# Kernel optimization log

Measured on AMD Instinct MI355X. Metric: run time of the kernel, lower is better.

## Reference

```python
import jax, jax.numpy as jnp
import numpy as np

RF = 8.0            # reduction_factor
NITER = 3           # k_means_iterations
FWHM = 128.0
TEMP_S = 0.066
TEMP_T = 0.033
MAX_DIST = 4.0
SIGMA2 = (FWHM / 2.355) ** 2


def _norm(x):
    # F.normalize(p=2, dim=-1) with eps=1e-12
    n = jnp.linalg.norm(x, axis=-1, keepdims=True)
    return x / jnp.maximum(n, 1e-12)


def _resize_axis(x, axis, out_size):
    # Linear resample along one axis with align_corners=False half-pixel
    # convention; equivalent to identity-affine grid_sample (coords stay
    # in-bounds for downsampling, so reflection padding never triggers).
    S = x.shape[axis]
    src = (jnp.arange(out_size, dtype=jnp.float32) + 0.5) * (S / out_size) - 0.5
    i0 = jnp.floor(src)
    w = src - i0
    i0c = jnp.clip(i0.astype(jnp.int32), 0, S - 1)
    i1c = jnp.clip(i0c + 1, 0, S - 1)
    x0 = jnp.take(x, i0c, axis=axis)
    x1 = jnp.take(x, i1c, axis=axis)
    shp = [1] * x.ndim
    shp[axis] = out_size
    w = w.reshape(shp)
    return x0 * (1.0 - w) + x1 * w


def _sample(emb, coord, reduction, jitter=None):
    # reduced size computed from ORIGINAL shape (before jitter crop)
    reduced = [max(int(s // reduction), 1) for s in emb.shape[2:]]
    if jitter is not None:
        j = jitter
        emb = emb[:, :, j[0]:emb.shape[2] - j[1], j[2]:emb.shape[3] - j[3], j[4]:emb.shape[4] - j[5]]
        coord = coord[:, :, j[0]:coord.shape[2] - j[1], j[2]:coord.shape[3] - j[3], j[4]:coord.shape[4] - j[5]]
    for ax, r in zip((2, 3, 4), reduced):
        emb = _resize_axis(emb, ax, r)
        coord = _resize_axis(coord, ax, r)
    b, c = emb.shape[:2]
    emb_flat = emb.reshape(b, c, -1).transpose(0, 2, 1)  # b n c
    return emb_flat, coord  # coord kept 5D: b 3 h w d


def _sqdist(cx, cy):
    # squared pairwise distance between flattened coord volumes: (b, Nx, Ny)
    b = cx.shape[0]
    x = cx.reshape(b, 3, -1)
    y = cy.reshape(b, 3, -1)
    d = x[:, :, :, None] - y[:, :, None, :]
    return jnp.sum(d * d, axis=1)


def _cluster(emb_p, coord_p, emb_t, coord_t):
    emb_t_n = _norm(emb_t)
    emb_p_n = _norm(emb_p)
    b = emb_t.shape[0]
    hp, wp, dp = coord_p.shape[2:]
    coord_t_flat = coord_t.reshape(b, 3, -1).transpose(0, 2, 1)  # b n 3
    for _ in range(NITER):
        sim = jax.nn.softmax(jnp.einsum('bnc,bpc->bnp', emb_t_n, emb_p_n) / TEMP_T, axis=-1)
        w = sim * jnp.exp(-_sqdist(coord_t, coord_p) / (2.0 * SIGMA2))
        denom = jnp.sum(w, axis=1)[:, :, None]  # b p 1
        emb_p = jnp.einsum('bnp,bnc->bpc', w, emb_t) / denom
        emb_p_n = _norm(emb_p)
        cp = jnp.einsum('bnp,bnc->bpc', w, coord_t_flat) / denom  # b p 3
        coord_p = cp.transpose(0, 2, 1).reshape(b, 3, hp, wp, dp)
    sim = jax.nn.softmax(jnp.einsum('bnc,bpc->bnp', emb_t_n, emb_p_n) / TEMP_T, axis=-1)
    w = sim * jnp.exp(-_sqdist(coord_t, coord_p) / (2.0 * SIGMA2))
    return emb_p, coord_p, w


def _assign(emb_z, coord_z, coord_t, emb_p, sim_t_p):
    emb_z_n = _norm(emb_z)
    emb_p_n = _norm(emb_p)
    # nearest-teacher assignment (non-differentiable in torch too)
    d = jnp.sqrt(_sqdist(jax.lax.stop_gradient(coord_z), jax.lax.stop_gradient(coord_t)))  # b Nz Nt
    pos_min = jnp.min(d, axis=-1)
    idx = jnp.argmin(d, axis=-1)                       # b Nz
    mask = (pos_min <= MAX_DIST).astype(emb_z.dtype)    # b Nz
    sim_soft = jax.nn.softmax(jnp.einsum('bnc,bpc->bnp', emb_z_n, emb_p_n) / TEMP_S, axis=-1)
    assignment = jnp.take_along_axis(sim_t_p, idx[:, :, None], axis=1)  # b Nz P
    logterm = jnp.clip(jnp.log(sim_soft + 1e-16), -1000.0, 0.0)
    rows = -jnp.sum(assignment * logterm, axis=-1)      # b Nz
    return jnp.sum(rows * mask, axis=1) / jnp.sum(mask, axis=1)  # (b,)


def setup_inputs() -> dict:
    key = jax.random.key(0)
    k1, k2 = jax.random.split(key)
    B, C, H, W, D = 2, 64, 80, 80, 80
    emb_s = jax.random.normal(k1, (B, C, H, W, D), dtype=jnp.float32)
    emb_t = jax.random.normal(k2, (B, C, H, W, D), dtype=jnp.float32)
    ax = jnp.arange(H, dtype=jnp.float32)
    mesh = jnp.stack(jnp.meshgrid(ax, ax, ax, indexing='ij'), axis=0)  # 3 h w d
    coord = jnp.broadcast_to(mesh[None], (B, 3, H, W, D)).astype(jnp.float32)
    return {"emb_s": emb_s, "emb_t": emb_t, "coord_s": coord, "coord_t": coord}


def reference(emb_s, emb_t, coord_s, coord_t):
    # jitter (torch: randint(0, ceil(rf), 6) under no_grad) -> static ints
    jit = np.random.default_rng(0).integers(0, int(np.ceil(RF)), 6)
    emb_p0, coord_p0 = _sample(emb_t, coord_t, RF * 2)
    emb_ts, coord_ts = _sample(emb_t, coord_t, RF)
    emb_ss, coord_ss = _sample(emb_s, coord_s, RF, jitter=jit)
    emb_p, coord_p, sim_t_p = _cluster(emb_p0, coord_p0, emb_ts, coord_ts)
    per_b = _assign(emb_ss, coord_ss, coord_ts, emb_p, sim_t_p)
    return jnp.mean(per_b)
```

## Files before the change

kernel.cpp:

```cpp
#include <hip/hip_runtime.h>
#include <stdint.h>
#include <stddef.h>


namespace {

constexpr int kB = 2;
constexpr int kNT = 1000, kNP = 125, kNZ = 1000;
constexpr float kTempT = 0.033f, kTempS = 0.066f;
constexpr double kSig2 = (128.0 / 2.355) * (128.0 / 2.355);
constexpr float kTwoSig2 = (float)(2.0 * kSig2);

struct Pcg64 {
  __uint128_t state, inc;
  static __uint128_t mult() {
    return (((__uint128_t)2549297995355413924ULL) << 64) | 4865540595714422341ULL;
  }
  void step() { state = state * mult() + inc; }
  void seed(__uint128_t initstate, __uint128_t initseq) {
    state = 0; inc = (initseq << 1) | 1; step(); state += initstate; step();
  }
  uint64_t next64() {
    step();
    uint64_t xo = (uint64_t)(state >> 64) ^ (uint64_t)state;
    unsigned rot = (unsigned)((uint64_t)(state >> 122) & 63u);
    return (xo >> rot) | (xo << ((64u - rot) & 63u));
  }
};

static inline uint32_t ss_hashmix(uint32_t v, uint32_t& hc) {
  v ^= hc; hc *= 0x931e8875u; v *= hc; v ^= v >> 16; return v;
}
static inline uint32_t ss_mix(uint32_t x, uint32_t y) {
  uint32_t r = (0xca01f9ddu * x) ^ (0x4973f715u * y);
  r ^= r >> 16; return r;
}

static void numpy_jitter_seed0(int jit[6]) {
  uint32_t pool[4];
  uint32_t hc = 0x43b0d7e5u;
  for (int i = 0; i < 4; ++i) pool[i] = ss_hashmix(0u, hc);
  for (int s = 0; s < 4; ++s)
    for (int d = 0; d < 4; ++d)
      if (s != d) pool[d] = ss_mix(pool[d], ss_hashmix(pool[s], hc));
  uint32_t w32[8];
  uint32_t hb = 0x8b51f9ddu;
  for (int i = 0; i < 8; ++i) {
    uint32_t dv = pool[i & 3];
    dv ^= hb; hb *= 0x58f38dedu; dv *= hb; dv ^= dv >> 16;
    w32[i] = dv;
  }
  uint64_t w64[4];
  for (int i = 0; i < 4; ++i)
    w64[i] = (uint64_t)w32[2 * i] | ((uint64_t)w32[2 * i + 1] << 32);
  Pcg64 rng;
  rng.seed((((__uint128_t)w64[0]) << 64) | w64[1],
           (((__uint128_t)w64[2]) << 64) | w64[3]);
  for (int i = 0; i < 6; ++i) jit[i] = (int)(rng.next64() & 7ULL);
}


struct AxisTap { int a, b; float w; };

__device__ inline AxisTap axis_tap(int i, float sc, int S) {
  float src = (i + 0.5f) * sc - 0.5f;
  float f = floorf(src);
  float w = src - f;
  int a = (int)f; a = a < 0 ? 0 : (a > S - 1 ? S - 1 : a);
  int b = (a + 1 > S - 1) ? S - 1 : a + 1;
  return {a, b, w};
}

__device__ inline float trilerp_vals(float v000, float v100, float v010, float v110,
                                     float v001, float v101, float v011, float v111,
                                     float w0, float w1, float w2) {
  float t00 = v000 * (1.0f - w0) + v100 * w0;
  float t10 = v010 * (1.0f - w0) + v110 * w0;
  float t01 = v001 * (1.0f - w0) + v101 * w0;
  float t11 = v011 * (1.0f - w0) + v111 * w0;
  float u0 = t00 * (1.0f - w1) + t10 * w1;
  float u1 = t01 * (1.0f - w1) + t11 * w1;
  return u0 * (1.0f - w2) + u1 * w2;
}

__device__ inline void coord_exact(int i, int j, int k,
                                   float sc0, float sc1, float sc2,
                                   int s0, int s1, int s2, int S0, int S1, int S2,
                                   float& c0o, float& c1o, float& c2o) {
#pragma clang fp contract(off)
  float src0 = (i + 0.5f) * sc0 - 0.5f;
  float f0 = floorf(src0); float w0 = src0 - f0;
  int a0 = (int)f0; a0 = a0 < 0 ? 0 : (a0 > S0 - 1 ? S0 - 1 : a0);
  int b0 = (a0 + 1 > S0 - 1) ? S0 - 1 : a0 + 1;

  float src1 = (j + 0.5f) * sc1 - 0.5f;
  float f1 = floorf(src1); float w1 = src1 - f1;
  int a1 = (int)f1; a1 = a1 < 0 ? 0 : (a1 > S1 - 1 ? S1 - 1 : a1);
  int b1 = (a1 + 1 > S1 - 1) ? S1 - 1 : a1 + 1;

  float src2 = (k + 0.5f) * sc2 - 0.5f;
  float f2 = floorf(src2); float w2 = src2 - f2;
  int a2 = (int)f2; a2 = a2 < 0 ? 0 : (a2 > S2 - 1 ? S2 - 1 : a2);
  int b2 = (a2 + 1 > S2 - 1) ? S2 - 1 : a2 + 1;

  float v0 = (float)(s0 + a0), v1 = (float)(s0 + b0);
  float c0 = v0 * (1.0f - w0) + v1 * w0;
  c0 = c0 * (1.0f - w1) + c0 * w1;
  c0 = c0 * (1.0f - w2) + c0 * w2;

  float g0 = (float)(s1 + a1), g1 = (float)(s1 + b1);
  float gA = g0 * (1.0f - w0) + g0 * w0;
  float gB = g1 * (1.0f - w0) + g1 * w0;
  float c1 = gA * (1.0f - w1) + gB * w1;
  c1 = c1 * (1.0f - w2) + c1 * w2;

  float h0 = (float)(s2 + a2), h1 = (float)(s2 + b2);
  float hA = h0 * (1.0f - w0) + h0 * w0;
  float hB = h1 * (1.0f - w0) + h1 * w0;
  hA = hA * (1.0f - w1) + hA * w1;
  hB = hB * (1.0f - w1) + hB * w1;
  float c2 = hA * (1.0f - w2) + hB * w2;

  c0o = c0; c1o = c1; c2o = c2;
}

__device__ inline void argmin_rowT(float zx, float zy, float zz,
                                   const float* ct0, const float* ct1, const float* ct2,
                                   int lane, float& best, int& bidx) {
#pragma clang fp contract(off)
  best = 3.4e38f; bidx = 0x7fffffff;
  for (int i = 0; i < 16; ++i) {
    float dx = zx - ct0[i * 64 + lane];
    float dy = zy - ct1[i * 64 + lane];
    float dz = zz - ct2[i * 64 + lane];
    float q0 = dx * dx, q1 = dy * dy, q2 = dz * dz;
    float d = sqrtf((q0 + q1) + q2);
    int n = lane * 16 + i;
    if (d < best) { best = d; bidx = n; }
  }
  for (int o = 32; o; o >>= 1) {
    float ob = __shfl_xor(best, o, 64);
    int oi = __shfl_xor(bidx, o, 64);
    if (ob < best || (ob == best && oi < bidx)) { best = ob; bidx = oi; }
  }
}


__global__ __launch_bounds__(256) void sampler_kernel(
    const float* __restrict__ emb_t, const float* __restrict__ emb_s,
    float* __restrict__ EMB_TS, float* __restrict__ EMB_TN,
    float* __restrict__ EMB_ZN, float* __restrict__ EMB_PN,
    float* __restrict__ COORD_P, float* __restrict__ COORD_T,
    float* __restrict__ COORD_Z, int* __restrict__ cnt,
    int j0, int j2, int j4, int S0, int S1, int S2,
    float scZ0, float scZ1, float scZ2) {
  if (blockIdx.x == 0 && threadIdx.x == 0) atomicExch(cnt, 0);
  __shared__ float tile[4][20][64];
  __shared__ int zg[20];

  int blk = blockIdx.x;
  int fam, b, i, jj, Kb;
  float sc0, sc1, sc2; int Sa0, Sa1, Sa2, o0, o1, o2;
  const float* src;
  if (blk < 50) {
    fam = 0; int r = blk; b = r / 25; r %= 25; i = r / 5; jj = r % 5; Kb = 5;
    sc0 = sc1 = sc2 = 16.0f; Sa0 = Sa1 = Sa2 = 80; o0 = o1 = o2 = 0; src = emb_t;
  } else if (blk < 250) {
    fam = 1; int r = blk - 50; b = r / 100; r %= 100; i = r / 10; jj = r % 10; Kb = 10;
    sc0 = sc1 = sc2 = 8.0f; Sa0 = Sa1 = Sa2 = 80; o0 = o1 = o2 = 0; src = emb_t;
  } else {
    fam = 2; int r = blk - 250; b = r / 100; r %= 100; i = r / 10; jj = r % 10; Kb = 10;
    sc0 = scZ0; sc1 = scZ1; sc2 = scZ2; Sa0 = S0; Sa1 = S1; Sa2 = S2;
    o0 = j0; o1 = j2; o2 = j4; src = emb_s;
  }
  AxisTap t0 = axis_tap(i, sc0, Sa0);
  AxisTap t1 = axis_tap(jj, sc1, Sa1);
  if (threadIdx.x < (unsigned)(2 * Kb)) {
    AxisTap tz = axis_tap((int)threadIdx.x >> 1, sc2, Sa2);
    zg[threadIdx.x] = o2 + ((threadIdx.x & 1) ? tz.b : tz.a);
  }
  __syncthreads();
  int wv = threadIdx.x >> 6, lane = threadIdx.x & 63;
  {
    int dx = wv >> 1, dy = wv & 1;
    int x = o0 + (dx ? t0.b : t0.a);
    int y = o1 + (dy ? t1.b : t1.a);
    int chq = lane & 15, zseg = lane >> 4;
    size_t xyoff = ((size_t)x * 80 + y) * 80;
    for (int chg = 0; chg < 4; ++chg) {
      int ch = chg * 16 + chq;
      const float* row = src + ((size_t)(b * 64 + ch)) * 512000 + xyoff;
      for (int zi = zseg; zi < 2 * Kb; zi += 4) tile[wv][zi][ch] = row[zg[zi]];
    }
  }
  __syncthreads();

  for (int k = wv; k < Kb; k += 4) {
    AxisTap t2 = axis_tap(k, sc2, Sa2);
    int z0 = 2 * k, z1 = 2 * k + 1;
    float v000 = tile[0][z0][lane], v001 = tile[0][z1][lane];
    float v010 = tile[1][z0][lane], v011 = tile[1][z1][lane];
    float v100 = tile[2][z0][lane], v101 = tile[2][z1][lane];
    float v110 = tile[3][z0][lane], v111 = tile[3][z1][lane];
    float x = trilerp_vals(v000, v100, v010, v110, v001, v101, v011, v111,
                           t0.w, t1.w, t2.w);
    float ss = x * x;
    for (int o = 32; o; o >>= 1) ss += __shfl_xor(ss, o, 64);
    float nrm = sqrtf(ss);
    float xn = x / fmaxf(nrm, 1e-12f);

    if (fam == 0) {
      int p = (i * 5 + jj) * 5 + k;
      EMB_PN[((size_t)b * kNP + p) * 64 + lane] = xn;
      if (lane == 0) {
        float c0, c1, c2;
        coord_exact(i, jj, k, 16.0f, 16.0f, 16.0f, 0, 0, 0, 80, 80, 80, c0, c1, c2);
        size_t o3 = ((size_t)b * kNP + p) * 3;
        COORD_P[o3] = c0; COORD_P[o3 + 1] = c1; COORD_P[o3 + 2] = c2;
      }
    } else if (fam == 1) {
      int n = (i * 10 + jj) * 10 + k;
      EMB_TS[((size_t)b * kNT + n) * 64 + lane] = x;
      EMB_TN[((size_t)b * kNT + n) * 64 + lane] = xn;
      if (lane == 0) {
        float c0, c1, c2;
        coord_exact(i, jj, k, 8.0f, 8.0f, 8.0f, 0, 0, 0, 80, 80, 80, c0, c1, c2);
        size_t o3 = ((size_t)b * kNT + n) * 3;
        COORD_T[o3] = c0; COORD_T[o3 + 1] = c1; COORD_T[o3 + 2] = c2;
      }
    } else {
      int n = (i * 10 + jj) * 10 + k;
      EMB_ZN[((size_t)b * kNZ + n) * 64 + lane] = xn;
      if (lane == 0) {
        float c0, c1, c2;
        coord_exact(i, jj, k, scZ0, scZ1, scZ2, j0, j2, j4, S0, S1, S2, c0, c1, c2);
        size_t o3 = ((size_t)b * kNZ + n) * 3;
        COORD_Z[o3] = c0; COORD_Z[o3 + 1] = c1; COORD_Z[o3 + 2] = c2;
      }
    }
  }
}

__global__ __launch_bounds__(256) void wkernel(
    const float* __restrict__ embtn, const float* __restrict__ embpn,
    const float* __restrict__ coordt, const float* __restrict__ coordp,
    float* __restrict__ W) {
  __shared__ float pnT[64 * 129];
  __shared__ float en[8][64];
  __shared__ float cpx[128], cpy[128], cpz[128];
  int b = blockIdx.x / 125, grp = blockIdx.x % 125;
  for (int t = threadIdx.x; t < kNP * 64; t += 256) {
    int p = t >> 6, c = t & 63;
    pnT[c * 129 + p] = embpn[((size_t)b * kNP + p) * 64 + c];
  }
  for (int t = threadIdx.x; t < kNP; t += 256) {
    cpx[t] = coordp[((size_t)b * kNP + t) * 3 + 0];
    cpy[t] = coordp[((size_t)b * kNP + t) * 3 + 1];
    cpz[t] = coordp[((size_t)b * kNP + t) * 3 + 2];
  }
  for (int t = threadIdx.x; t < 8 * 64; t += 256) {
    int r = t >> 6, c = t & 63;
    en[r][c] = embtn[((size_t)b * kNT + grp * 8 + r) * 64 + c];
  }
  __syncthreads();
  int wv = threadIdx.x >> 6, lane = threadIdx.x & 63;
  bool v1 = lane < (kNP - 64);
  for (int rr = wv; rr < 8; rr += 4) {
    int n = grp * 8 + rr;
    float a0 = 0.f, a1 = 0.f;
#pragma unroll
    for (int c = 0; c < 64; ++c) {
      float ec = en[rr][c];
      a0 += ec * pnT[c * 129 + lane];
      a1 += ec * pnT[c * 129 + 64 + lane];
    }
    float l0 = a0 / kTempT;
    float l1 = v1 ? (a1 / kTempT) : -3.4e38f;
    float m = fmaxf(l0, l1);
    for (int o = 32; o; o >>= 1) m = fmaxf(m, __shfl_xor(m, o, 64));
    float e0 = expf(l0 - m);
    float e1 = v1 ? expf(l1 - m) : 0.f;
    float s = e0 + e1;
    for (int o = 32; o; o >>= 1) s += __shfl_xor(s, o, 64);
    float tx = coordt[((size_t)b * kNT + n) * 3 + 0];
    float ty = coordt[((size_t)b * kNT + n) * 3 + 1];
    float tz = coordt[((size_t)b * kNT + n) * 3 + 2];
    {
      float dx = tx - cpx[lane], dy = ty - cpy[lane], dz = tz - cpz[lane];
      float d2 = dx * dx + dy * dy + dz * dz;
      W[((size_t)b * kNT + n) * kNP + lane] = (e0 / s) * expf(-d2 / kTwoSig2);
    }
    if (v1) {
      float dx = tx - cpx[64 + lane], dy = ty - cpy[64 + lane], dz = tz - cpz[64 + lane];
      float d2 = dx * dx + dy * dy + dz * dz;
      W[((size_t)b * kNT + n) * kNP + 64 + lane] = (e1 / s) * expf(-d2 / kTwoSig2);
    }
  }
}

__global__ __launch_bounds__(256) void update_kernel(
    const float* __restrict__ W, const float* __restrict__ embts,
    const float* __restrict__ coordt, float* __restrict__ embpn,
    float* __restrict__ coordp) {
  int bp = blockIdx.x; int b = bp / kNP; int p = bp % kNP;
  int wv = threadIdx.x >> 6, lane = threadIdx.x & 63;
  __shared__ float wcol[kNT];
  const float* Wb = W + ((size_t)b * kNT) * kNP + p;
  for (int n = threadIdx.x; n < kNT; n += 256) wcol[n] = Wb[(size_t)n * kNP];
  __syncthreads();

  float accE = 0.f, accC = 0.f, accD = 0.f;
  const float* Eb = embts + ((size_t)b * kNT) * 64;
  const float* Cb = coordt + ((size_t)b * kNT) * 3;
#pragma unroll 2
  for (int n0 = wv * 250; n0 < (wv + 1) * 250; n0 += 10) {
    float w[10], e[10], cc[10];
#pragma unroll
    for (int u = 0; u < 10; ++u) w[u] = wcol[n0 + u];
#pragma unroll
    for (int u = 0; u < 10; ++u) e[u] = Eb[(size_t)(n0 + u) * 64 + lane];
    if (lane < 3) {
#pragma unroll
      for (int u = 0; u < 10; ++u) cc[u] = Cb[(size_t)(n0 + u) * 3 + lane];
    }
#pragma unroll
    for (int u = 0; u < 10; ++u) {
      accD += w[u];
      accE += w[u] * e[u];
      if (lane < 3) accC += w[u] * cc[u];
    }
  }
  __shared__ float sE[4][64];
  __shared__ float sC[4][3];
  __shared__ float sD[4];
  sE[wv][lane] = accE;
  if (lane < 3) sC[wv][lane] = accC;
  if (lane == 0) sD[wv] = accD;
  __syncthreads();
  if (threadIdx.x < 64) {
    float d = sD[0] + sD[1] + sD[2] + sD[3];
    float x = (sE[0][lane] + sE[1][lane] + sE[2][lane] + sE[3][lane]) / d;
    float ss = x * x;
    for (int o = 32; o; o >>= 1) ss += __shfl_xor(ss, o, 64);
    float nrm = sqrtf(ss);
    embpn[((size_t)b * kNP + p) * 64 + lane] = x / fmaxf(nrm, 1e-12f);
    if (lane < 3) {
      float cc2 = sC[0][lane] + sC[1][lane] + sC[2][lane] + sC[3][lane];
      coordp[((size_t)b * kNP + p) * 3 + lane] = cc2 / d;
    }
  }
}

__global__ __launch_bounds__(256) void loss_kernel(
    const float* __restrict__ embzn, const float* __restrict__ embtn,
    const float* __restrict__ embpn, const float* __restrict__ coordz,
    const float* __restrict__ coordt, const float* __restrict__ coordp,
    float* __restrict__ partials, int* __restrict__ counter,
    float* __restrict__ out) {
  __shared__ float pnT[64 * 129];
  __shared__ float ctT0[1024], ctT1[1024], ctT2[1024];
  __shared__ float en[4][64];
  __shared__ float cpx[128], cpy[128], cpz[128];
  __shared__ float sR[4], sM[4];
  int b = blockIdx.x / 250, chunk = blockIdx.x % 250;
  for (int t = threadIdx.x; t < kNP * 64; t += 256) {
    int p = t >> 6, c = t & 63;
    pnT[c * 129 + p] = embpn[((size_t)b * kNP + p) * 64 + c];
  }
  for (int t = threadIdx.x; t < kNP; t += 256) {
    cpx[t] = coordp[((size_t)b * kNP + t) * 3 + 0];
    cpy[t] = coordp[((size_t)b * kNP + t) * 3 + 1];
    cpz[t] = coordp[((size_t)b * kNP + t) * 3 + 2];
  }
  for (int n = threadIdx.x; n < 1024; n += 256) {
    int pos = (n & 15) * 64 + (n >> 4);
    if (n < 1000) {
      ctT0[pos] = coordt[((size_t)b * kNT + n) * 3 + 0];
      ctT1[pos] = coordt[((size_t)b * kNT + n) * 3 + 1];
      ctT2[pos] = coordt[((size_t)b * kNT + n) * 3 + 2];
    } else {
      ctT0[pos] = 3.4e38f; ctT1[pos] = 3.4e38f; ctT2[pos] = 3.4e38f;
    }
  }
  {
    int r = threadIdx.x >> 6, c = threadIdx.x & 63;
    en[r][c] = embzn[((size_t)b * kNZ + chunk * 4 + r) * 64 + c];
  }
  __syncthreads();
  int wv = threadIdx.x >> 6, lane = threadIdx.x & 63;
  bool v1 = lane < (kNP - 64);
  int z = chunk * 4 + wv;

  float zx = coordz[((size_t)b * kNZ + z) * 3 + 0];
  float zy = coordz[((size_t)b * kNZ + z) * 3 + 1];
  float zzv = coordz[((size_t)b * kNZ + z) * 3 + 2];
  float best; int id;
  argmin_rowT(zx, zy, zzv, ctT0, ctT1, ctT2, lane, best, id);
  float msk = (best <= 4.0f) ? 1.0f : 0.0f;

  float a0 = 0.f, a1 = 0.f;
#pragma unroll
  for (int c = 0; c < 64; ++c) {
    float ec = en[wv][c];
    a0 += ec * pnT[c * 129 + lane];
    a1 += ec * pnT[c * 129 + 64 + lane];
  }
  float l0 = a0 / kTempS;
  float l1 = v1 ? (a1 / kTempS) : -3.4e38f;
  float m = fmaxf(l0, l1);
  for (int o = 32; o; o >>= 1) m = fmaxf(m, __shfl_xor(m, o, 64));
  float e0 = expf(l0 - m), e1 = v1 ? expf(l1 - m) : 0.f;
  float s = e0 + e1;
  for (int o = 32; o; o >>= 1) s += __shfl_xor(s, o, 64);
  float lt0 = fminf(fmaxf(logf(e0 / s + 1e-16f), -1000.0f), 0.0f);
  float lt1 = 0.f;
  if (v1) lt1 = fminf(fmaxf(logf(e1 / s + 1e-16f), -1000.0f), 0.0f);

  float ev = embtn[((size_t)b * kNT + id) * 64 + lane];
  float wa0 = 0.f, wa1 = 0.f;
#pragma unroll
  for (int c = 0; c < 64; ++c) {
    float ec = __shfl(ev, c, 64);
    wa0 += ec * pnT[c * 129 + lane];
    wa1 += ec * pnT[c * 129 + 64 + lane];
  }
  float wl0 = wa0 / kTempT;
  float wl1 = v1 ? (wa1 / kTempT) : -3.4e38f;
  float wm = fmaxf(wl0, wl1);
  for (int o = 32; o; o >>= 1) wm = fmaxf(wm, __shfl_xor(wm, o, 64));
  float we0 = expf(wl0 - wm);
  float we1 = v1 ? expf(wl1 - wm) : 0.f;
  float wsum = we0 + we1;
  for (int o = 32; o; o >>= 1) wsum += __shfl_xor(wsum, o, 64);
  int pos = (id & 15) * 64 + (id >> 4);
  float tx = ctT0[pos], ty = ctT1[pos], tz = ctT2[pos];
  float W0, W1 = 0.f;
  {
    float dx = tx - cpx[lane], dy = ty - cpy[lane], dz = tz - cpz[lane];
    float d2 = dx * dx + dy * dy + dz * dz;
    W0 = (we0 / wsum) * expf(-d2 / kTwoSig2);
  }
  if (v1) {
    float dx = tx - cpx[64 + lane], dy = ty - cpy[64 + lane], dz = tz - cpz[64 + lane];
    float d2 = dx * dx + dy * dy + dz * dz;
    W1 = (we1 / wsum) * expf(-d2 / kTwoSig2);
  }

  float r = W0 * lt0;
  if (v1) r += W1 * lt1;
  for (int o = 32; o; o >>= 1) r += __shfl_xor(r, o, 64);
  if (lane == 0) { sR[wv] = -(r * msk); sM[wv] = msk; }
  __syncthreads();
  if (threadIdx.x == 0) {
    partials[(size_t)(b * 250 + chunk) * 2 + 0] = sR[0] + sR[1] + sR[2] + sR[3];
    partials[(size_t)(b * 250 + chunk) * 2 + 1] = sM[0] + sM[1] + sM[2] + sM[3];
  }
  __syncthreads();
  __shared__ int isLast;
  if (threadIdx.x == 0) {
    __threadfence();
    isLast = (atomicAdd(counter, 1) == 499) ? 1 : 0;
  }
  __syncthreads();
  if (isLast && threadIdx.x < 64) {
    __threadfence();
    float loss = 0.f;
    for (int bb = 0; bb < kB; ++bb) {
      float rr = 0.f, mm = 0.f;
      for (int c2 = threadIdx.x; c2 < 250; c2 += 64) {
        rr += partials[(size_t)(bb * 250 + c2) * 2 + 0];
        mm += partials[(size_t)(bb * 250 + c2) * 2 + 1];
      }
      for (int o = 32; o; o >>= 1) {
        rr += __shfl_xor(rr, o, 64);
        mm += __shfl_xor(mm, o, 64);
      }
      loss += rr / mm;
    }
    if (threadIdx.x == 0) out[0] = loss * 0.5f;
  }
}

}

extern "C" void kernel_launch(void* const* d_in, const int* in_sizes, int n_in,
                              void* d_out, int out_size, void* d_ws, size_t ws_size,
                              hipStream_t stream) {
  (void)in_sizes; (void)n_in; (void)out_size; (void)ws_size;
  const float* emb_s = (const float*)d_in[0];
  const float* emb_t = (const float*)d_in[1];

  float* ws = (float*)d_ws;
  float* EMB_TS  = ws + 0;
  float* EMB_TN  = ws + 128000;
  float* EMB_ZN  = ws + 256000;
  float* EMB_PN  = ws + 384000;
  float* COORD_P = ws + 400000;
  float* COORD_T = ws + 400752;
  float* COORD_Z = ws + 406752;
  float* Wbuf    = ws + 412752;
  float* PART    = ws + 662752;
  int*   CNT     = (int*)(ws + 663752);

  int jit[6];
  numpy_jitter_seed0(jit);
  int S0 = 80 - jit[0] - jit[1];
  int S1 = 80 - jit[2] - jit[3];
  int S2 = 80 - jit[4] - jit[5];
  float scZ0 = (float)(S0 / 10.0);
  float scZ1 = (float)(S1 / 10.0);
  float scZ2 = (float)(S2 / 10.0);

  sampler_kernel<<<450, 256, 0, stream>>>(
      emb_t, emb_s, EMB_TS, EMB_TN, EMB_ZN, EMB_PN, COORD_P, COORD_T, COORD_Z,
      CNT, jit[0], jit[2], jit[4], S0, S1, S2, scZ0, scZ1, scZ2);

  for (int it = 0; it < 3; ++it) {
    wkernel<<<250, 256, 0, stream>>>(EMB_TN, EMB_PN, COORD_T, COORD_P, Wbuf);
    update_kernel<<<250, 256, 0, stream>>>(Wbuf, EMB_TS, COORD_T, EMB_PN, COORD_P);
  }

  loss_kernel<<<500, 256, 0, stream>>>(EMB_ZN, EMB_TN, EMB_PN, COORD_Z, COORD_T,
                                       COORD_P, PART, CNT, (float*)d_out);
}
```

Measured before the change: 109.8 us.

## Split sampler into per-channel gather stage and trilinear interpolation stage

The single sampler kernel, which gathered 8 corner taps for 64 channels per spatial point, is replaced by two kernels. The first gathers the needed voxel taps for each (batch, channel) plane into compact 20^3 and 10^3 buffers in workspace. The second runs one wave per output point, doing trilinear interpolation with float2 loads plus normalisation. This aims to make the strided global gathers from the large input volumes more localised per channel, at the cost of an extra kernel launch and a round trip through an intermediate buffer of several MB.

```diff
diff --git a/kernel.cpp b/kernel.cpp
--- a/kernel.cpp
+++ b/kernel.cpp
@@ -146,97 +146,133 @@
 }
 
 
-__global__ __launch_bounds__(256) void sampler_kernel(
+__global__ __launch_bounds__(256) void stageA_kernel(
     const float* __restrict__ emb_t, const float* __restrict__ emb_s,
+    float* __restrict__ Bt, float* __restrict__ Bp, float* __restrict__ Bs,
+    int* __restrict__ cnt,
+    int j0, int j2, int j4, int S0, int S1, int S2,
+    float scZ0, float scZ1, float scZ2) {
+  if (blockIdx.x == 0 && threadIdx.x == 0) atomicExch(cnt, 0);
+  __shared__ int xt[20], yt[20], zt[20];
+  __shared__ int xp[10];
+  int idx = blockIdx.x;
+  bool isT = idx < 128;
+  int r = isT ? idx : idx - 128;
+  int b = r >> 6, ch = r & 63;
+
+  if (isT) {
+    if (threadIdx.x < 20) {
+      AxisTap t = axis_tap((int)threadIdx.x >> 1, 8.0f, 80);
+      int v = (threadIdx.x & 1) ? t.b : t.a;
+      xt[threadIdx.x] = v; yt[threadIdx.x] = v; zt[threadIdx.x] = v;
+    }
+    if (threadIdx.x < 10) {
+      AxisTap t = axis_tap((int)threadIdx.x >> 1, 16.0f, 80);
+      xp[threadIdx.x] = (threadIdx.x & 1) ? t.b : t.a;
+    }
+  } else {
+    if (threadIdx.x < 20) {
+      int h = (int)threadIdx.x >> 1, odd = threadIdx.x & 1;
+      AxisTap tx0 = axis_tap(h, scZ0, S0);
+      AxisTap ty0 = axis_tap(h, scZ1, S1);
+      AxisTap tz0 = axis_tap(h, scZ2, S2);
+      xt[threadIdx.x] = j0 + (odd ? tx0.b : tx0.a);
+      yt[threadIdx.x] = j2 + (odd ? ty0.b : ty0.a);
+      zt[threadIdx.x] = j4 + (odd ? tz0.b : tz0.a);
+    }
+  }
+  __syncthreads();
+
+  const float* src = (isT ? emb_t : emb_s) + ((size_t)(b * 64 + ch)) * 512000;
+  float* dstT = (isT ? Bt : Bs) + ((size_t)(b * 64 + ch)) * 8000;
+
+#pragma unroll 4
+  for (int e = threadIdx.x; e < 8000; e += 256) {
+    int zi = e % 20; int rr = e / 20; int yi = rr % 20; int xi = rr / 20;
+    dstT[e] = src[((size_t)xt[xi] * 80 + yt[yi]) * 80 + zt[zi]];
+  }
+  if (isT) {
+    float* dstP = Bp + ((size_t)(b * 64 + ch)) * 1000;
+#pragma unroll 4
+    for (int e = threadIdx.x; e < 1000; e += 256) {
+      int zi = e % 10; int rr = e / 10; int yi = rr % 10; int xi = rr / 10;
+      dstP[e] = src[((size_t)xp[xi] * 80 + xp[yi]) * 80 + xp[zi]];
+    }
+  }
+}
+
+__global__ __launch_bounds__(256) void stageB_kernel(
+    const float* __restrict__ Bt, const float* __restrict__ Bp,
+    const float* __restrict__ Bs,
     float* __restrict__ EMB_TS, float* __restrict__ EMB_TN,
     float* __restrict__ EMB_ZN, float* __restrict__ EMB_PN,
     float* __restrict__ COORD_P, float* __restrict__ COORD_T,
-    float* __restrict__ COORD_Z, int* __restrict__ cnt,
+    float* __restrict__ COORD_Z,
     int j0, int j2, int j4, int S0, int S1, int S2,
     float scZ0, float scZ1, float scZ2) {
-  if (blockIdx.x == 0 && threadIdx.x == 0) atomicExch(cnt, 0);
-  __shared__ float tile[4][20][64];
-  __shared__ int zg[20];
-
-  int blk = blockIdx.x;
-  int fam, b, i, jj, Kb;
-  float sc0, sc1, sc2; int Sa0, Sa1, Sa2, o0, o1, o2;
-  const float* src;
-  if (blk < 50) {
-    fam = 0; int r = blk; b = r / 25; r %= 25; i = r / 5; jj = r % 5; Kb = 5;
-    sc0 = sc1 = sc2 = 16.0f; Sa0 = Sa1 = Sa2 = 80; o0 = o1 = o2 = 0; src = emb_t;
-  } else if (blk < 250) {
-    fam = 1; int r = blk - 50; b = r / 100; r %= 100; i = r / 10; jj = r % 10; Kb = 10;
-    sc0 = sc1 = sc2 = 8.0f; Sa0 = Sa1 = Sa2 = 80; o0 = o1 = o2 = 0; src = emb_t;
-  } else {
-    fam = 2; int r = blk - 250; b = r / 100; r %= 100; i = r / 10; jj = r % 10; Kb = 10;
-    sc0 = scZ0; sc1 = scZ1; sc2 = scZ2; Sa0 = S0; Sa1 = S1; Sa2 = S2;
-    o0 = j0; o1 = j2; o2 = j4; src = emb_s;
-  }
-  AxisTap t0 = axis_tap(i, sc0, Sa0);
-  AxisTap t1 = axis_tap(jj, sc1, Sa1);
-  if (threadIdx.x < (unsigned)(2 * Kb)) {
-    AxisTap tz = axis_tap((int)threadIdx.x >> 1, sc2, Sa2);
-    zg[threadIdx.x] = o2 + ((threadIdx.x & 1) ? tz.b : tz.a);
-  }
-  __syncthreads();
-  int wv = threadIdx.x >> 6, lane = threadIdx.x & 63;
-  {
-    int dx = wv >> 1, dy = wv & 1;
-    int x = o0 + (dx ? t0.b : t0.a);
-    int y = o1 + (dy ? t1.b : t1.a);
-    int chq = lane & 15, zseg = lane >> 4;
-    size_t xyoff = ((size_t)x * 80 + y) * 80;
-    for (int chg = 0; chg < 4; ++chg) {
-      int ch = chg * 16 + chq;
-      const float* row = src + ((size_t)(b * 64 + ch)) * 512000 + xyoff;
-      for (int zi = zseg; zi < 2 * Kb; zi += 4) tile[wv][zi][ch] = row[zg[zi]];
-    }
-  }
-  __syncthreads();
-
-  for (int k = wv; k < Kb; k += 4) {
-    AxisTap t2 = axis_tap(k, sc2, Sa2);
-    int z0 = 2 * k, z1 = 2 * k + 1;
-    float v000 = tile[0][z0][lane], v001 = tile[0][z1][lane];
-    float v010 = tile[1][z0][lane], v011 = tile[1][z1][lane];
-    float v100 = tile[2][z0][lane], v101 = tile[2][z1][lane];
-    float v110 = tile[3][z0][lane], v111 = tile[3][z1][lane];
-    float x = trilerp_vals(v000, v100, v010, v110, v001, v101, v011, v111,
+  int wid = blockIdx.x * 4 + (threadIdx.x >> 6);
+  int lane = threadIdx.x & 63;
+  if (wid >= 4250) return;
+
+  if (wid < 250) {
+    int b = wid / 125, p = wid % 125;
+    int i = p / 25, jj = (p / 5) % 5, k = p % 5;
+    AxisTap t0 = axis_tap(i, 16.0f, 80), t1 = axis_tap(jj, 16.0f, 80), t2 = axis_tap(k, 16.0f, 80);
+    const float2* base = (const float2*)(Bp + ((size_t)(b * 64 + lane)) * 1000) +
+                         (i * 100 + jj * 10 + k);
+    float2 c00 = base[0], c01 = base[5], c10 = base[50], c11 = base[55];
+    float x = trilerp_vals(c00.x, c10.x, c01.x, c11.x, c00.y, c10.y, c01.y, c11.y,
                            t0.w, t1.w, t2.w);
     float ss = x * x;
     for (int o = 32; o; o >>= 1) ss += __shfl_xor(ss, o, 64);
     float nrm = sqrtf(ss);
-    float xn = x / fmaxf(nrm, 1e-12f);
-
-    if (fam == 0) {
-      int p = (i * 5 + jj) * 5 + k;
-      EMB_PN[((size_t)b * kNP + p) * 64 + lane] = xn;
-      if (lane == 0) {
-        float c0, c1, c2;
-        coord_exact(i, jj, k, 16.0f, 16.0f, 16.0f, 0, 0, 0, 80, 80, 80, c0, c1, c2);
-        size_t o3 = ((size_t)b * kNP + p) * 3;
-        COORD_P[o3] = c0; COORD_P[o3 + 1] = c1; COORD_P[o3 + 2] = c2;
-      }
-    } else if (fam == 1) {
-      int n = (i * 10 + jj) * 10 + k;
-      EMB_TS[((size_t)b * kNT + n) * 64 + lane] = x;
-      EMB_TN[((size_t)b * kNT + n) * 64 + lane] = xn;
-      if (lane == 0) {
-        float c0, c1, c2;
-        coord_exact(i, jj, k, 8.0f, 8.0f, 8.0f, 0, 0, 0, 80, 80, 80, c0, c1, c2);
-        size_t o3 = ((size_t)b * kNT + n) * 3;
-        COORD_T[o3] = c0; COORD_T[o3 + 1] = c1; COORD_T[o3 + 2] = c2;
-      }
-    } else {
-      int n = (i * 10 + jj) * 10 + k;
-      EMB_ZN[((size_t)b * kNZ + n) * 64 + lane] = xn;
-      if (lane == 0) {
-        float c0, c1, c2;
-        coord_exact(i, jj, k, scZ0, scZ1, scZ2, j0, j2, j4, S0, S1, S2, c0, c1, c2);
-        size_t o3 = ((size_t)b * kNZ + n) * 3;
-        COORD_Z[o3] = c0; COORD_Z[o3 + 1] = c1; COORD_Z[o3 + 2] = c2;
-      }
+    EMB_PN[((size_t)b * kNP + p) * 64 + lane] = x / fmaxf(nrm, 1e-12f);
+    if (lane == 0) {
+      float c0, c1, c2;
+      coord_exact(i, jj, k, 16.0f, 16.0f, 16.0f, 0, 0, 0, 80, 80, 80, c0, c1, c2);
+      size_t o3 = ((size_t)b * kNP + p) * 3;
+      COORD_P[o3] = c0; COORD_P[o3 + 1] = c1; COORD_P[o3 + 2] = c2;
+    }
+  } else if (wid < 2250) {
+    int idx = wid - 250;
+    int b = idx / 1000, n = idx % 1000;
+    int i = n / 100, jj = (n / 10) % 10, k = n % 10;
+    AxisTap t0 = axis_tap(i, 8.0f, 80), t1 = axis_tap(jj, 8.0f, 80), t2 = axis_tap(k, 8.0f, 80);
+    const float2* base = (const float2*)(Bt + ((size_t)(b * 64 + lane)) * 8000) +
+                         (i * 400 + jj * 20 + k);
+    float2 c00 = base[0], c01 = base[10], c10 = base[200], c11 = base[210];
+    float x = trilerp_vals(c00.x, c10.x, c01.x, c11.x, c00.y, c10.y, c01.y, c11.y,
+                           t0.w, t1.w, t2.w);
+    EMB_TS[((size_t)b * kNT + n) * 64 + lane] = x;
+    float ss = x * x;
+    for (int o = 32; o; o >>= 1) ss += __shfl_xor(ss, o, 64);
+    float nrm = sqrtf(ss);
+    EMB_TN[((size_t)b * kNT + n) * 64 + lane] = x / fmaxf(nrm, 1e-12f);
+    if (lane == 0) {
+      float c0, c1, c2;
+      coord_exact(i, jj, k, 8.0f, 8.0f, 8.0f, 0, 0, 0, 80, 80, 80, c0, c1, c2);
+      size_t o3 = ((size_t)b * kNT + n) * 3;
+      COORD_T[o3] = c0; COORD_T[o3 + 1] = c1; COORD_T[o3 + 2] = c2;
+    }
+  } else {
+    int idx = wid - 2250;
+    int b = idx / 1000, n = idx % 1000;
+    int i = n / 100, jj = (n / 10) % 10, k = n % 10;
+    AxisTap t0 = axis_tap(i, scZ0, S0), t1 = axis_tap(jj, scZ1, S1), t2 = axis_tap(k, scZ2, S2);
+    const float2* base = (const float2*)(Bs + ((size_t)(b * 64 + lane)) * 8000) +
+                         (i * 400 + jj * 20 + k);
+    float2 c00 = base[0], c01 = base[10], c10 = base[200], c11 = base[210];
+    float x = trilerp_vals(c00.x, c10.x, c01.x, c11.x, c00.y, c10.y, c01.y, c11.y,
+                           t0.w, t1.w, t2.w);
+    float ss = x * x;
+    for (int o = 32; o; o >>= 1) ss += __shfl_xor(ss, o, 64);
+    float nrm = sqrtf(ss);
+    EMB_ZN[((size_t)b * kNZ + n) * 64 + lane] = x / fmaxf(nrm, 1e-12f);
+    if (lane == 0) {
+      float c0, c1, c2;
+      coord_exact(i, jj, k, scZ0, scZ1, scZ2, j0, j2, j4, S0, S1, S2, c0, c1, c2);
+      size_t o3 = ((size_t)b * kNZ + n) * 3;
+      COORD_Z[o3] = c0; COORD_Z[o3 + 1] = c1; COORD_Z[o3 + 2] = c2;
     }
   }
 }
@@ -491,16 +527,19 @@
   const float* emb_t = (const float*)d_in[1];
 
   float* ws = (float*)d_ws;
-  float* EMB_TS  = ws + 0;
-  float* EMB_TN  = ws + 128000;
-  float* EMB_ZN  = ws + 256000;
-  float* EMB_PN  = ws + 384000;
-  float* COORD_P = ws + 400000;
-  float* COORD_T = ws + 400752;
-  float* COORD_Z = ws + 406752;
-  float* Wbuf    = ws + 412752;
-  float* PART    = ws + 662752;
-  int*   CNT     = (int*)(ws + 663752);
+  float* Bt      = ws + 0;
+  float* Bs      = ws + 1024000;
+  float* Bp      = ws + 2048000;
+  float* EMB_TS  = ws + 2176000;
+  float* EMB_TN  = ws + 2304000;
+  float* EMB_ZN  = ws + 2432000;
+  float* EMB_PN  = ws + 2560000;
+  float* COORD_P = ws + 2576000;
+  float* COORD_T = ws + 2576752;
+  float* COORD_Z = ws + 2582752;
+  float* Wbuf    = ws + 2588752;
+  float* PART    = ws + 2838752;
+  int*   CNT     = (int*)(ws + 2839752);
 
   int jit[6];
   numpy_jitter_seed0(jit);
@@ -511,9 +550,13 @@
   float scZ1 = (float)(S1 / 10.0);
   float scZ2 = (float)(S2 / 10.0);
 
-  sampler_kernel<<<450, 256, 0, stream>>>(
-      emb_t, emb_s, EMB_TS, EMB_TN, EMB_ZN, EMB_PN, COORD_P, COORD_T, COORD_Z,
-      CNT, jit[0], jit[2], jit[4], S0, S1, S2, scZ0, scZ1, scZ2);
+  stageA_kernel<<<256, 256, 0, stream>>>(
+      emb_t, emb_s, Bt, Bp, Bs, CNT, jit[0], jit[2], jit[4], S0, S1, S2,
+      scZ0, scZ1, scZ2);
+
+  stageB_kernel<<<(4250 + 3) / 4, 256, 0, stream>>>(
+      Bt, Bp, Bs, EMB_TS, EMB_TN, EMB_ZN, EMB_PN, COORD_P, COORD_T, COORD_Z,
+      jit[0], jit[2], jit[4], S0, S1, S2, scZ0, scZ1, scZ2);
 
   for (int it = 0; it < 3; ++it) {
     wkernel<<<250, 256, 0, stream>>>(EMB_TN, EMB_PN, COORD_T, COORD_P, Wbuf);
```

Result: slower. 114.5 us (+4.3%).
